# Kernel tuning notes

Measured on AMD Instinct MI355X. Metric: run time of the kernel, lower is better.

Reference implementation:

```python
import jax, jax.numpy as jnp
import numpy as np

N_NODES, N_EDGES, N_GRAPHS = 20000, 320000, 64
D_IN, D_H, D_FC, OUT_DIMS = 1280, 512, 1024, 5000
BN_EPS = 1e-5


def setup_inputs() -> dict:
    key = jax.random.key(0)
    ks = jax.random.split(key, 12)
    sc = lambda k, s: (jax.random.normal(k, s, jnp.float32) * 0.02)
    return {
        "x": jax.random.normal(ks[0], (N_NODES, D_IN), jnp.float32),
        "edge_index": jax.random.randint(ks[1], (2, N_EDGES), 0, N_NODES, dtype=jnp.int64),
        "batch": jnp.sort(jax.random.randint(ks[2], (N_NODES,), 0, N_GRAPHS, dtype=jnp.int64)),
        "Wg1": sc(ks[3], (D_IN, D_H)),
        "bg1": jnp.zeros((D_H,), jnp.float32),
        "Wg2": sc(ks[4], (D_H, D_H)),
        "bg2": jnp.zeros((D_H,), jnp.float32),
        "W1": sc(ks[5], (D_H, D_FC)),
        "b1": jnp.zeros((D_FC,), jnp.float32),
        "W2": sc(ks[6], (D_FC, OUT_DIMS)),
        "b2": jnp.zeros((OUT_DIMS,), jnp.float32),
        "gamma": jnp.ones((OUT_DIMS,), jnp.float32),
        "beta": jnp.zeros((OUT_DIMS,), jnp.float32),
    }


def _gcn_conv(h_in, W, b, src, dst):
    # PyG GCNConv: linear transform, symmetric deg^{-1/2} normalization with self-loops.
    h = h_in @ W  # [N, D]
    ones = jnp.ones((src.shape[0],), h.dtype)
    deg = jax.ops.segment_sum(ones, dst, num_segments=N_NODES) + 1.0  # self-loop
    dinv = jax.lax.rsqrt(deg)  # [N]
    coef = dinv[src] * dinv[dst]  # [E]
    agg = jax.ops.segment_sum(h[src] * coef[:, None], dst, num_segments=N_NODES)
    agg = agg + h * (dinv * dinv)[:, None]  # self-loop contribution
    return agg + b


def reference(x, edge_index, batch, Wg1, bg1, Wg2, bg2, W1, b1, W2, b2, gamma, beta):
    src, dst = edge_index[0], edge_index[1]
    h = jax.nn.relu(_gcn_conv(x, Wg1, bg1, src, dst))
    h = jax.nn.relu(_gcn_conv(h, Wg2, bg2, src, dst))
    # global max pool over each graph in the batch
    g = jax.ops.segment_max(h, batch, num_segments=N_GRAPHS)  # [G, 512]
    # fc head (eval mode: dropout = identity, BatchNorm1d uses running stats mean=0, var=1)
    h1 = jax.nn.relu(g @ W1 + b1)
    logits = h1 @ W2 + b2
    bn = logits * (gamma / jnp.sqrt(1.0 + BN_EPS)) + beta
    return jax.nn.sigmoid(bn)
```

## Files before the change

kernel.cpp:

```cpp
#include <hip/hip_runtime.h>
#include <math.h>

#define N_NODES 20000
#define N_EDGES 320000
#define N_GRAPHS 64
#define D_IN 1280
#define D_H 512
#define D_FC 1024
#define OUT_DIMS 5000

typedef unsigned short ushort_t;
typedef short bf16x8 __attribute__((ext_vector_type(8)));
typedef float f32x4 __attribute__((ext_vector_type(4)));

__device__ __forceinline__ ushort_t f2b(float x) {
    unsigned u = __float_as_uint(x);
    unsigned r = (u + 0x7FFFu + ((u >> 16) & 1u)) >> 16;
    return (ushort_t)r;
}

#define GLL16(gp, lp)                                                                  \
    __builtin_amdgcn_global_load_lds((const __attribute__((address_space(1))) void*)(gp), \
                                     (__attribute__((address_space(3))) void*)(lp), 16, 0, 0)

#define CONV_SWIZZLE()                                         \
    const int f = blockIdx.y * 32 + blockIdx.x;                \
    const int rt = (f >> 5) * 8 + (f & 7);                     \
    const int ct = (f & 31) >> 3;                              \
    const int rowBase = rt * 128;                              \
    const int colBase = ct * 128;                              \
    if (rowBase >= M) return;

__global__ __launch_bounds__(256) void mfma_gemm_db(const ushort_t* __restrict__ A,
                                                    const ushort_t* __restrict__ BT,
                                                    ushort_t* __restrict__ C,
                                                    int M, int N, int K) {
    __shared__ ushort_t lds[4 * 4096];
    const int t = threadIdx.x;
    const int lane = t & 63, wave = t >> 6;
    const int wrow = (wave >> 1) * 64, wcol = (wave & 1) * 64;
    const int lo = lane & 15, quad = lane >> 4;
    CONV_SWIZZLE();

    const int s0 = t, s1 = t + 256;
    const int r0 = s0 >> 2, r1 = s1 >> 2;
    const int q0 = (s0 & 3) ^ ((r0 >> 1) & 3);
    const int q1 = (s1 & 3) ^ ((r1 >> 1) & 3);
    int ar0 = rowBase + r0; if (ar0 >= M) ar0 = M - 1;
    int ar1 = rowBase + r1; if (ar1 >= M) ar1 = M - 1;
    const ushort_t* pa0 = A + (size_t)ar0 * K + q0 * 8;
    const ushort_t* pa1 = A + (size_t)ar1 * K + q1 * 8;
    const ushort_t* pb0 = BT + (size_t)(colBase + r0) * K + q0 * 8;
    const ushort_t* pb1 = BT + (size_t)(colBase + r1) * K + q1 * 8;

#define ISSUE_TILE(p)                                                  \
    {                                                                  \
        GLL16(pa0, lds + (p) * 4096 + wave * 512);                     \
        GLL16(pa1, lds + (p) * 4096 + 2048 + wave * 512);              \
        GLL16(pb0, lds + 8192 + (p) * 4096 + wave * 512);              \
        GLL16(pb1, lds + 8192 + (p) * 4096 + 2048 + wave * 512);       \
        pa0 += 32; pa1 += 32; pb0 += 32; pb1 += 32;                    \
    }

    const int qs = (quad ^ ((lo >> 1) & 3)) * 8;
    int offA[4], offB[4];
#pragma unroll
    for (int i = 0; i < 4; ++i) offA[i] = (wrow + i * 16 + lo) * 32 + qs;
#pragma unroll
    for (int j = 0; j < 4; ++j) offB[j] = (wcol + j * 16 + lo) * 32 + qs;

    f32x4 acc[4][4] = {};
    const int NK = K >> 5;

    ISSUE_TILE(0);
    if (NK > 1) ISSUE_TILE(1);

    for (int k = 0; k < NK; ++k) {
        __syncthreads();
        const ushort_t* Ab = lds + (k & 1) * 4096;
        const ushort_t* Bb = lds + 8192 + (k & 1) * 4096;
        bf16x8 af[4], bfr[4];
#pragma unroll
        for (int i = 0; i < 4; ++i) af[i] = *(const bf16x8*)&Ab[offA[i]];
#pragma unroll
        for (int j = 0; j < 4; ++j) bfr[j] = *(const bf16x8*)&Bb[offB[j]];
        __syncthreads();
        if (k + 2 < NK) ISSUE_TILE(k & 1);
#pragma unroll
        for (int i = 0; i < 4; ++i)
#pragma unroll
            for (int j = 0; j < 4; ++j)
                acc[i][j] = __builtin_amdgcn_mfma_f32_16x16x32_bf16(af[i], bfr[j], acc[i][j], 0, 0, 0);
    }
#undef ISSUE_TILE

#pragma unroll
    for (int i = 0; i < 4; ++i) {
        int row0 = rowBase + wrow + i * 16 + quad * 4;
#pragma unroll
        for (int j = 0; j < 4; ++j) {
            int col = colBase + wcol + j * 16 + lo;
            if (col >= N) continue;
#pragma unroll
            for (int r = 0; r < 4; ++r) {
                int row = row0 + r;
                if (row < M) C[(size_t)row * N + col] = f2b(acc[i][j][r]);
            }
        }
    }
}

__global__ void cvt_f32_bf16(const float* __restrict__ X, ushort_t* __restrict__ Y, int n8) {
    int i = blockIdx.x * blockDim.x + threadIdx.x;
    if (i >= n8) return;
    const float4* p = (const float4*)(X + (size_t)i * 8);
    float4 v0 = p[0], v1 = p[1];
    ushort_t w[8] = {f2b(v0.x), f2b(v0.y), f2b(v0.z), f2b(v0.w),
                     f2b(v1.x), f2b(v1.y), f2b(v1.z), f2b(v1.w)};
    *(uint4*)(Y + (size_t)i * 8) = *(uint4*)w;
}

__global__ void wt_cvt_transpose(const float* __restrict__ W, ushort_t* __restrict__ WT,
                                 int K, int N) {
    int i = blockIdx.x * blockDim.x + threadIdx.x;
    if (i >= N * K) return;
    int n = i / K, k = i - n * K;
    WT[i] = f2b(W[(size_t)k * N + n]);
}

__global__ __launch_bounds__(256) void gemm_splitk(const float* __restrict__ A,
                                                   const float* __restrict__ B,
                                                   float* __restrict__ P,
                                                   int M, int N, int K, int KC) {
    __shared__ float As[16][64];
    __shared__ float Bs[16][64];
    const int t = threadIdx.x;
    const int tx = t & 15, ty = t >> 4;
    const int rowBase = blockIdx.y * 64;
    const int colBase = blockIdx.x * 64;
    const int kbeg = blockIdx.z * KC;
    const int kend = kbeg + KC;
    float acc[4][4] = {};
    for (int k0 = kbeg; k0 < kend; k0 += 16) {
#pragma unroll
        for (int i = 0; i < 4; ++i) {
            int idx = t + i * 256;
            int row = idx >> 4, kk = idx & 15;
            int gr = rowBase + row;
            As[kk][row] = (gr < M) ? A[(size_t)gr * K + k0 + kk] : 0.f;
        }
#pragma unroll
        for (int i = 0; i < 4; ++i) {
            int idx = t + i * 256;
            int kk = idx >> 6, col = idx & 63;
            int gc = colBase + col;
            Bs[kk][col] = (gc < N) ? B[(size_t)(k0 + kk) * N + gc] : 0.f;
        }
        __syncthreads();
#pragma unroll
        for (int kk = 0; kk < 16; ++kk) {
            float a[4], b[4];
#pragma unroll
            for (int i = 0; i < 4; ++i) a[i] = As[kk][ty * 4 + i];
#pragma unroll
            for (int j = 0; j < 4; ++j) b[j] = Bs[kk][tx * 4 + j];
#pragma unroll
            for (int i = 0; i < 4; ++i)
#pragma unroll
                for (int j = 0; j < 4; ++j) acc[i][j] = fmaf(a[i], b[j], acc[i][j]);
        }
        __syncthreads();
    }
    float* Pz = P + (size_t)blockIdx.z * M * N;
#pragma unroll
    for (int i = 0; i < 4; ++i) {
        int gr = rowBase + ty * 4 + i;
        if (gr >= M) continue;
#pragma unroll
        for (int j = 0; j < 4; ++j) {
            int gc = colBase + tx * 4 + j;
            if (gc < N) Pz[(size_t)gr * N + gc] = acc[i][j];
        }
    }
}

__global__ void reduce_bias_relu(const float* __restrict__ P, const float* __restrict__ b,
                                 float* __restrict__ out, int total, int N, int S) {
    int i = blockIdx.x * blockDim.x + threadIdx.x;
    if (i >= total) return;
    float s = 0.f;
    for (int z = 0; z < S; ++z) s += P[(size_t)z * total + i];
    out[i] = fmaxf(s + b[i % N], 0.f);
}

__global__ void reduce_bn_sigmoid(const float* __restrict__ P, const float* __restrict__ b2,
                                  const float* __restrict__ gamma, const float* __restrict__ beta,
                                  float* __restrict__ out, int S) {
    int i = blockIdx.x * blockDim.x + threadIdx.x;
    if (i >= N_GRAPHS * OUT_DIMS) return;
    int c = i % OUT_DIMS;
    float s = 0.f;
    for (int z = 0; z < S; ++z) s += P[(size_t)z * N_GRAPHS * OUT_DIMS + i];
    const float sc = 0.9999950000374997f;
    float zz = (s + b2[c]) * (gamma[c] * sc) + beta[c];
    out[i] = 1.f / (1.f + expf(-zz));
}

__global__ void hist_deg(const int* __restrict__ dst, int* __restrict__ cnt) {
    int e = blockIdx.x * blockDim.x + threadIdx.x;
    if (e < N_EDGES) atomicAdd(cnt + dst[e], 1);
}

__global__ void compute_dinv(const int* __restrict__ cnt, float* __restrict__ dinv) {
    int v = blockIdx.x * blockDim.x + threadIdx.x;
    if (v < N_NODES) dinv[v] = rsqrtf((float)cnt[v] + 1.0f);
}

__global__ __launch_bounds__(256) void scan_rowptr(const int* __restrict__ cnt,
                                                   int* __restrict__ rowptr) {
    __shared__ int sums[256];
    const int t = threadIdx.x;
    const int CH = (N_NODES + 255) / 256;
    const int base = t * CH;
    int s = 0;
    for (int i = 0; i < CH; ++i) {
        int v = base + i;
        if (v < N_NODES) s += cnt[v];
    }
    sums[t] = s;
    __syncthreads();
    for (int off = 1; off < 256; off <<= 1) {
        int y = (t >= off) ? sums[t - off] : 0;
        __syncthreads();
        sums[t] += y;
        __syncthreads();
    }
    int run = sums[t] - s;
    for (int i = 0; i < CH; ++i) {
        int v = base + i;
        if (v < N_NODES) {
            rowptr[v] = run;
            run += cnt[v];
        }
    }
    if (t == 255) rowptr[N_NODES] = run;
}

__global__ void fill_csr(const int* __restrict__ src, const int* __restrict__ dst,
                         const int* __restrict__ rowptr, int* __restrict__ cursor,
                         int* __restrict__ col) {
    int e = blockIdx.x * blockDim.x + threadIdx.x;
    if (e < N_EDGES) {
        int d = dst[e];
        int p = rowptr[d] + atomicAdd(cursor + d, 1);
        col[p] = src[e];
    }
}

__device__ __forceinline__ void bf8_fma(uint4 v, float c, float* acc) {
    unsigned a[4] = {v.x, v.y, v.z, v.w};
#pragma unroll
    for (int i = 0; i < 4; ++i) {
        float lo = __uint_as_float(a[i] << 16);
        float hi = __uint_as_float(a[i] & 0xFFFF0000u);
        acc[2 * i]     = fmaf(lo, c, acc[2 * i]);
        acc[2 * i + 1] = fmaf(hi, c, acc[2 * i + 1]);
    }
}

__device__ __forceinline__ void agg_node_bf16(const ushort_t* __restrict__ H,
                                              const int* __restrict__ rowptr,
                                              const int* __restrict__ col,
                                              const float* __restrict__ dinv,
                                              const float* __restrict__ bias,
                                              int v, int f, float* r) {
    const int beg = rowptr[v], end = rowptr[v + 1];
    const float dv = dinv[v];
    float acc[8] = {};
    int j = beg;
    for (; j + 3 < end; j += 4) {
        int s0 = col[j], s1 = col[j + 1], s2 = col[j + 2], s3 = col[j + 3];
        float c0 = dinv[s0] * dv, c1 = dinv[s1] * dv;
        float c2 = dinv[s2] * dv, c3 = dinv[s3] * dv;
        uint4 h0 = *(const uint4*)(H + (size_t)s0 * D_H + f);
        uint4 h1 = *(const uint4*)(H + (size_t)s1 * D_H + f);
        uint4 h2 = *(const uint4*)(H + (size_t)s2 * D_H + f);
        uint4 h3 = *(const uint4*)(H + (size_t)s3 * D_H + f);
        bf8_fma(h0, c0, acc);
        bf8_fma(h1, c1, acc);
        bf8_fma(h2, c2, acc);
        bf8_fma(h3, c3, acc);
    }
    for (; j < end; ++j) {
        int s0 = col[j];
        float c0 = dinv[s0] * dv;
        uint4 h0 = *(const uint4*)(H + (size_t)s0 * D_H + f);
        bf8_fma(h0, c0, acc);
    }
    uint4 hv = *(const uint4*)(H + (size_t)v * D_H + f);
    bf8_fma(hv, dv * dv, acc);
    float4 b0 = *(const float4*)(bias + f);
    float4 b1 = *(const float4*)(bias + f + 4);
    r[0] = fmaxf(acc[0] + b0.x, 0.f);
    r[1] = fmaxf(acc[1] + b0.y, 0.f);
    r[2] = fmaxf(acc[2] + b0.z, 0.f);
    r[3] = fmaxf(acc[3] + b0.w, 0.f);
    r[4] = fmaxf(acc[4] + b1.x, 0.f);
    r[5] = fmaxf(acc[5] + b1.y, 0.f);
    r[6] = fmaxf(acc[6] + b1.z, 0.f);
    r[7] = fmaxf(acc[7] + b1.w, 0.f);
}

__global__ __launch_bounds__(64) void gather_agg_relu_bf16(const ushort_t* __restrict__ H,
                                                           const int* __restrict__ rowptr,
                                                           const int* __restrict__ col,
                                                           const float* __restrict__ dinv,
                                                           const float* __restrict__ bias,
                                                           ushort_t* __restrict__ out) {
    const int v = blockIdx.x;
    const int f = threadIdx.x * 8;
    float r[8];
    agg_node_bf16(H, rowptr, col, dinv, bias, v, f, r);
    ushort_t o[8];
#pragma unroll
    for (int i = 0; i < 8; ++i) o[i] = f2b(r[i]);
    *(uint4*)(out + (size_t)v * D_H + f) = *(uint4*)o;
}

__global__ void graph_bounds(const int* __restrict__ batch, int* __restrict__ gstart) {
    int g = threadIdx.x;
    if (g > N_GRAPHS) return;
    int lo = 0, hi = N_NODES;
    while (lo < hi) {
        int mid = (lo + hi) >> 1;
        if (batch[mid] < g) lo = mid + 1; else hi = mid;
    }
    gstart[g] = lo;
}

__global__ __launch_bounds__(64) void pool_max_seg(const ushort_t* __restrict__ h2,
                                                   const int* __restrict__ gstart,
                                                   float* __restrict__ gbuf) {
    const int g = blockIdx.x;
    const int f = blockIdx.y * 128 + threadIdx.x * 2;
    const int beg = gstart[g], end = gstart[g + 1];
    float m0 = -INFINITY, m1 = -INFINITY;
    int v = beg;
    for (; v + 3 < end; v += 4) {
        unsigned u0 = *(const unsigned*)(h2 + (size_t)(v + 0) * D_H + f);
        unsigned u1 = *(const unsigned*)(h2 + (size_t)(v + 1) * D_H + f);
        unsigned u2 = *(const unsigned*)(h2 + (size_t)(v + 2) * D_H + f);
        unsigned u3 = *(const unsigned*)(h2 + (size_t)(v + 3) * D_H + f);
        m0 = fmaxf(m0, fmaxf(fmaxf(__uint_as_float(u0 << 16), __uint_as_float(u1 << 16)),
                             fmaxf(__uint_as_float(u2 << 16), __uint_as_float(u3 << 16))));
        m1 = fmaxf(m1, fmaxf(fmaxf(__uint_as_float(u0 & 0xFFFF0000u), __uint_as_float(u1 & 0xFFFF0000u)),
                             fmaxf(__uint_as_float(u2 & 0xFFFF0000u), __uint_as_float(u3 & 0xFFFF0000u))));
    }
    for (; v < end; ++v) {
        unsigned u = *(const unsigned*)(h2 + (size_t)v * D_H + f);
        m0 = fmaxf(m0, __uint_as_float(u << 16));
        m1 = fmaxf(m1, __uint_as_float(u & 0xFFFF0000u));
    }
    gbuf[g * D_H + f] = m0;
    gbuf[g * D_H + f + 1] = m1;
}

extern "C" void kernel_launch(void* const* d_in, const int* in_sizes, int n_in,
                              void* d_out, int out_size, void* d_ws, size_t ws_size,
                              hipStream_t stream) {
    const float* x     = (const float*)d_in[0];
    const int*   ei    = (const int*)d_in[1];
    const int*   batch = (const int*)d_in[2];
    const float* Wg1   = (const float*)d_in[3];
    const float* bg1   = (const float*)d_in[4];
    const float* Wg2   = (const float*)d_in[5];
    const float* bg2   = (const float*)d_in[6];
    const float* W1    = (const float*)d_in[7];
    const float* b1    = (const float*)d_in[8];
    const float* W2    = (const float*)d_in[9];
    const float* b2    = (const float*)d_in[10];
    const float* gamma = (const float*)d_in[11];
    const float* beta  = (const float*)d_in[12];
    const int* src = ei;
    const int* dst = ei + N_EDGES;
    float* out = (float*)d_out;

    const int S1 = 4;
    const int S2 = 8;

    ushort_t* hpre   = (ushort_t*)d_ws;
    ushort_t* h1b    = hpre + (size_t)N_NODES * D_H;
    ushort_t* w1t    = h1b + (size_t)N_NODES * D_H;
    ushort_t* w2t    = w1t + (size_t)D_H * D_IN;
    ushort_t* xb     = w2t + (size_t)D_H * D_H;
    float*    dinv   = (float*)(xb + (size_t)N_NODES * D_IN);
    float*    gbuf   = dinv + N_NODES;
    float*    fc1o   = gbuf + N_GRAPHS * D_H;
    float*    part1  = fc1o + N_GRAPHS * D_FC;
    float*    part2  = part1 + (size_t)S1 * N_GRAPHS * D_FC;
    int*      cnt    = (int*)(part2 + (size_t)S2 * N_GRAPHS * OUT_DIMS);
    int*      rowptr = cnt + N_NODES;
    int*      cursor = rowptr + N_NODES + 1;
    int*      colidx = cursor + N_NODES;
    int*      gstart = colidx + N_EDGES;

    hipMemsetAsync(cnt, 0, N_NODES * sizeof(int), stream);
    hipMemsetAsync(cursor, 0, N_NODES * sizeof(int), stream);
    hist_deg<<<(N_EDGES + 255) / 256, 256, 0, stream>>>(dst, cnt);
    compute_dinv<<<(N_NODES + 255) / 256, 256, 0, stream>>>(cnt, dinv);
    scan_rowptr<<<1, 256, 0, stream>>>(cnt, rowptr);
    fill_csr<<<(N_EDGES + 255) / 256, 256, 0, stream>>>(src, dst, rowptr, cursor, colidx);
    wt_cvt_transpose<<<(D_H * D_IN + 255) / 256, 256, 0, stream>>>(Wg1, w1t, D_IN, D_H);
    wt_cvt_transpose<<<(D_H * D_H + 255) / 256, 256, 0, stream>>>(Wg2, w2t, D_H, D_H);
    cvt_f32_bf16<<<(N_NODES * D_IN / 8 + 255) / 256, 256, 0, stream>>>(x, xb, N_NODES * D_IN / 8);
    graph_bounds<<<1, N_GRAPHS + 1, 0, stream>>>(batch, gstart);

    dim3 gconv(32, 20);

    mfma_gemm_db<<<gconv, 256, 0, stream>>>(xb, w1t, hpre, N_NODES, D_H, D_IN);
    gather_agg_relu_bf16<<<N_NODES, 64, 0, stream>>>(hpre, rowptr, colidx, dinv, bg1, h1b);

    mfma_gemm_db<<<gconv, 256, 0, stream>>>(h1b, w2t, hpre, N_NODES, D_H, D_H);
    gather_agg_relu_bf16<<<N_NODES, 64, 0, stream>>>(hpre, rowptr, colidx, dinv, bg2, h1b);
    pool_max_seg<<<dim3(N_GRAPHS, 4), 64, 0, stream>>>(h1b, gstart, gbuf);

    dim3 gfc1((D_FC + 63) / 64, 1, S1);
    gemm_splitk<<<gfc1, 256, 0, stream>>>(gbuf, W1, part1, N_GRAPHS, D_FC, D_H, D_H / S1);
    reduce_bias_relu<<<(N_GRAPHS * D_FC + 255) / 256, 256, 0, stream>>>(
        part1, b1, fc1o, N_GRAPHS * D_FC, D_FC, S1);

    dim3 gfc2((OUT_DIMS + 63) / 64, 1, S2);
    gemm_splitk<<<gfc2, 256, 0, stream>>>(fc1o, W2, part2, N_GRAPHS, OUT_DIMS, D_FC, D_FC / S2);
    reduce_bn_sigmoid<<<(N_GRAPHS * OUT_DIMS + 255) / 256, 256, 0, stream>>>(
        part2, b2, gamma, beta, out, S2);
}
```

Measured before the change: 522.4 us.

## Fuse preprocessing kernels, tile weight transpose, and batch nodes per gather block

Merges the memsets, weight transposes, x conversion and graph-bounds search into one multi-role prep kernel, and folds the dinv computation into the scan kernel. This cuts the number of launches. The weight transpose now goes through a shared-memory tile so both reads and writes are coalesced. The gather and pool kernels use 256-thread blocks covering four nodes or a whole graph, and the fc1 split-K factor goes from 4 to 8. The cost is a more complex prep kernel whose roles are selected by block index, and a larger fc1 partial buffer.

```diff
diff --git a/kernel.cpp b/kernel.cpp
--- a/kernel.cpp
+++ b/kernel.cpp
@@ -110,22 +110,74 @@
     }
 }
 
-__global__ void cvt_f32_bf16(const float* __restrict__ X, ushort_t* __restrict__ Y, int n8) {
-    int i = blockIdx.x * blockDim.x + threadIdx.x;
-    if (i >= n8) return;
-    const float4* p = (const float4*)(X + (size_t)i * 8);
-    float4 v0 = p[0], v1 = p[1];
-    ushort_t w[8] = {f2b(v0.x), f2b(v0.y), f2b(v0.z), f2b(v0.w),
-                     f2b(v1.x), f2b(v1.y), f2b(v1.z), f2b(v1.w)};
-    *(uint4*)(Y + (size_t)i * 8) = *(uint4*)w;
-}
-
-__global__ void wt_cvt_transpose(const float* __restrict__ W, ushort_t* __restrict__ WT,
-                                 int K, int N) {
-    int i = blockIdx.x * blockDim.x + threadIdx.x;
-    if (i >= N * K) return;
-    int n = i / K, k = i - n * K;
-    WT[i] = f2b(W[(size_t)k * N + n]);
+#define PREP_ZB 10
+#define PREP_T1 640
+#define PREP_T2 256
+#define PREP_XB 12500
+#define PREP_NBLK (PREP_ZB + PREP_T1 + PREP_T2 + PREP_XB + 1)
+
+__global__ __launch_bounds__(256) void prep_all(const float* __restrict__ W1src, ushort_t* __restrict__ w1t,
+                                                const float* __restrict__ W2src, ushort_t* __restrict__ w2t,
+                                                const float* __restrict__ x, ushort_t* __restrict__ xb,
+                                                int* __restrict__ zbase,
+                                                const int* __restrict__ batch, int* __restrict__ gstart) {
+    __shared__ float tile[32][33];
+    int b = blockIdx.x;
+    const int t = threadIdx.x;
+
+    if (b < PREP_ZB) {
+        int i = b * 256 + t;
+        if (i < 2500) {
+            int4* p = (int4*)zbase + (size_t)i * 4;
+            int4 z = {0, 0, 0, 0};
+            p[0] = z; p[1] = z; p[2] = z; p[3] = z;
+        }
+        return;
+    }
+    b -= PREP_ZB;
+
+    if (b < PREP_T1 + PREP_T2) {
+        const float* W;
+        ushort_t* WT;
+        int K, N, tb;
+        if (b < PREP_T1) { W = W1src; WT = w1t; K = D_IN; N = D_H; tb = b; }
+        else             { W = W2src; WT = w2t; K = D_H;  N = D_H; tb = b - PREP_T1; }
+        const int ntn = N >> 5;
+        const int kt = tb / ntn, nt = tb - kt * ntn;
+        const int tx = t & 31, ty = t >> 5;
+#pragma unroll
+        for (int it = 0; it < 4; ++it) {
+            int k = kt * 32 + ty + it * 8;
+            tile[ty + it * 8][tx] = W[(size_t)k * N + nt * 32 + tx];
+        }
+        __syncthreads();
+#pragma unroll
+        for (int it = 0; it < 4; ++it) {
+            int n = nt * 32 + ty + it * 8;
+            WT[(size_t)n * K + kt * 32 + tx] = f2b(tile[tx][ty + it * 8]);
+        }
+        return;
+    }
+    b -= PREP_T1 + PREP_T2;
+
+    if (b < PREP_XB) {
+        int i = b * 256 + t;
+        const float4* p = (const float4*)(x + (size_t)i * 8);
+        float4 v0 = p[0], v1 = p[1];
+        ushort_t w[8] = {f2b(v0.x), f2b(v0.y), f2b(v0.z), f2b(v0.w),
+                         f2b(v1.x), f2b(v1.y), f2b(v1.z), f2b(v1.w)};
+        *(uint4*)(xb + (size_t)i * 8) = *(uint4*)w;
+        return;
+    }
+
+    if (t <= N_GRAPHS) {
+        int lo = 0, hi = N_NODES;
+        while (lo < hi) {
+            int mid = (lo + hi) >> 1;
+            if (batch[mid] < t) lo = mid + 1; else hi = mid;
+        }
+        gstart[t] = lo;
+    }
 }
 
 __global__ __launch_bounds__(256) void gemm_splitk(const float* __restrict__ A,
@@ -159,15 +211,15 @@
         __syncthreads();
 #pragma unroll
         for (int kk = 0; kk < 16; ++kk) {
-            float a[4], b[4];
+            float a[4], bb[4];
 #pragma unroll
             for (int i = 0; i < 4; ++i) a[i] = As[kk][ty * 4 + i];
 #pragma unroll
-            for (int j = 0; j < 4; ++j) b[j] = Bs[kk][tx * 4 + j];
+            for (int j = 0; j < 4; ++j) bb[j] = Bs[kk][tx * 4 + j];
 #pragma unroll
             for (int i = 0; i < 4; ++i)
 #pragma unroll
-                for (int j = 0; j < 4; ++j) acc[i][j] = fmaf(a[i], b[j], acc[i][j]);
+                for (int j = 0; j < 4; ++j) acc[i][j] = fmaf(a[i], bb[j], acc[i][j]);
         }
         __syncthreads();
     }
@@ -211,13 +263,9 @@
     if (e < N_EDGES) atomicAdd(cnt + dst[e], 1);
 }
 
-__global__ void compute_dinv(const int* __restrict__ cnt, float* __restrict__ dinv) {
-    int v = blockIdx.x * blockDim.x + threadIdx.x;
-    if (v < N_NODES) dinv[v] = rsqrtf((float)cnt[v] + 1.0f);
-}
-
-__global__ __launch_bounds__(256) void scan_rowptr(const int* __restrict__ cnt,
-                                                   int* __restrict__ rowptr) {
+__global__ __launch_bounds__(256) void scan_rowptr_dinv(const int* __restrict__ cnt,
+                                                        int* __restrict__ rowptr,
+                                                        float* __restrict__ dinv) {
     __shared__ int sums[256];
     const int t = threadIdx.x;
     const int CH = (N_NODES + 255) / 256;
@@ -225,7 +273,11 @@
     int s = 0;
     for (int i = 0; i < CH; ++i) {
         int v = base + i;
-        if (v < N_NODES) s += cnt[v];
+        if (v < N_NODES) {
+            int c = cnt[v];
+            s += c;
+            dinv[v] = rsqrtf((float)c + 1.0f);
+        }
     }
     sums[t] = s;
     __syncthreads();
@@ -311,14 +363,14 @@
     r[7] = fmaxf(acc[7] + b1.w, 0.f);
 }
 
-__global__ __launch_bounds__(64) void gather_agg_relu_bf16(const ushort_t* __restrict__ H,
-                                                           const int* __restrict__ rowptr,
-                                                           const int* __restrict__ col,
-                                                           const float* __restrict__ dinv,
-                                                           const float* __restrict__ bias,
-                                                           ushort_t* __restrict__ out) {
-    const int v = blockIdx.x;
-    const int f = threadIdx.x * 8;
+__global__ __launch_bounds__(256) void gather_agg_relu_bf16(const ushort_t* __restrict__ H,
+                                                            const int* __restrict__ rowptr,
+                                                            const int* __restrict__ col,
+                                                            const float* __restrict__ dinv,
+                                                            const float* __restrict__ bias,
+                                                            ushort_t* __restrict__ out) {
+    const int v = blockIdx.x * 4 + (threadIdx.x >> 6);
+    const int f = (threadIdx.x & 63) * 8;
     float r[8];
     agg_node_bf16(H, rowptr, col, dinv, bias, v, f, r);
     ushort_t o[8];
@@ -327,22 +379,11 @@
     *(uint4*)(out + (size_t)v * D_H + f) = *(uint4*)o;
 }
 
-__global__ void graph_bounds(const int* __restrict__ batch, int* __restrict__ gstart) {
-    int g = threadIdx.x;
-    if (g > N_GRAPHS) return;
-    int lo = 0, hi = N_NODES;
-    while (lo < hi) {
-        int mid = (lo + hi) >> 1;
-        if (batch[mid] < g) lo = mid + 1; else hi = mid;
-    }
-    gstart[g] = lo;
-}
-
-__global__ __launch_bounds__(64) void pool_max_seg(const ushort_t* __restrict__ h2,
-                                                   const int* __restrict__ gstart,
-                                                   float* __restrict__ gbuf) {
+__global__ __launch_bounds__(256) void pool_max_seg(const ushort_t* __restrict__ h2,
+                                                    const int* __restrict__ gstart,
+                                                    float* __restrict__ gbuf) {
     const int g = blockIdx.x;
-    const int f = blockIdx.y * 128 + threadIdx.x * 2;
+    const int f = threadIdx.x * 2;
     const int beg = gstart[g], end = gstart[g + 1];
     float m0 = -INFINITY, m1 = -INFINITY;
     int v = beg;
@@ -385,7 +426,7 @@
     const int* dst = ei + N_EDGES;
     float* out = (float*)d_out;
 
-    const int S1 = 4;
+    const int S1 = 8;
     const int S2 = 8;
 
     ushort_t* hpre   = (ushort_t*)d_ws;
@@ -399,30 +440,25 @@
     float*    part1  = fc1o + N_GRAPHS * D_FC;
     float*    part2  = part1 + (size_t)S1 * N_GRAPHS * D_FC;
     int*      cnt    = (int*)(part2 + (size_t)S2 * N_GRAPHS * OUT_DIMS);
-    int*      rowptr = cnt + N_NODES;
-    int*      cursor = rowptr + N_NODES + 1;
-    int*      colidx = cursor + N_NODES;
+    int*      cursor = cnt + N_NODES;
+    int*      rowptr = cursor + N_NODES;
+    int*      colidx = rowptr + N_NODES + 1;
     int*      gstart = colidx + N_EDGES;
 
-    hipMemsetAsync(cnt, 0, N_NODES * sizeof(int), stream);
-    hipMemsetAsync(cursor, 0, N_NODES * sizeof(int), stream);
+    prep_all<<<PREP_NBLK, 256, 0, stream>>>(Wg1, w1t, Wg2, w2t, x, xb, cnt, batch, gstart);
+
     hist_deg<<<(N_EDGES + 255) / 256, 256, 0, stream>>>(dst, cnt);
-    compute_dinv<<<(N_NODES + 255) / 256, 256, 0, stream>>>(cnt, dinv);
-    scan_rowptr<<<1, 256, 0, stream>>>(cnt, rowptr);
+    scan_rowptr_dinv<<<1, 256, 0, stream>>>(cnt, rowptr, dinv);
     fill_csr<<<(N_EDGES + 255) / 256, 256, 0, stream>>>(src, dst, rowptr, cursor, colidx);
-    wt_cvt_transpose<<<(D_H * D_IN + 255) / 256, 256, 0, stream>>>(Wg1, w1t, D_IN, D_H);
-    wt_cvt_transpose<<<(D_H * D_H + 255) / 256, 256, 0, stream>>>(Wg2, w2t, D_H, D_H);
-    cvt_f32_bf16<<<(N_NODES * D_IN / 8 + 255) / 256, 256, 0, stream>>>(x, xb, N_NODES * D_IN / 8);
-    graph_bounds<<<1, N_GRAPHS + 1, 0, stream>>>(batch, gstart);
 
     dim3 gconv(32, 20);
 
     mfma_gemm_db<<<gconv, 256, 0, stream>>>(xb, w1t, hpre, N_NODES, D_H, D_IN);
-    gather_agg_relu_bf16<<<N_NODES, 64, 0, stream>>>(hpre, rowptr, colidx, dinv, bg1, h1b);
+    gather_agg_relu_bf16<<<N_NODES / 4, 256, 0, stream>>>(hpre, rowptr, colidx, dinv, bg1, h1b);
 
     mfma_gemm_db<<<gconv, 256, 0, stream>>>(h1b, w2t, hpre, N_NODES, D_H, D_H);
-    gather_agg_relu_bf16<<<N_NODES, 64, 0, stream>>>(hpre, rowptr, colidx, dinv, bg2, h1b);
-    pool_max_seg<<<dim3(N_GRAPHS, 4), 64, 0, stream>>>(h1b, gstart, gbuf);
+    gather_agg_relu_bf16<<<N_NODES / 4, 256, 0, stream>>>(hpre, rowptr, colidx, dinv, bg2, h1b);
+    pool_max_seg<<<N_GRAPHS, 256, 0, stream>>>(h1b, gstart, gbuf);
 
     dim3 gfc1((D_FC + 63) / 64, 1, S1);
     gemm_splitk<<<gfc1, 256, 0, stream>>>(gbuf, W1, part1, N_GRAPHS, D_FC, D_H, D_H / S1);
```

Result: faster. 511.2 us (-2.1%).
